# Performance work log

Measured on AMD Instinct MI355X. Metric: run time of the kernel, lower is better.

Reference implementation:

```python
import jax, jax.numpy as jnp
import numpy as np

N = 100000
NEG_SLOPE = 0.2

def setup_inputs() -> dict:
    key = jax.random.key(0)
    ks = jax.random.split(key, 12)
    F_in, H, C1, C2 = 128, 2, 64, 64
    E = 1600000
    x = jax.random.normal(ks[0], (N, F_in), dtype=jnp.float32)
    edge_index = jax.random.randint(ks[1], (2, E), 0, N, dtype=jnp.int32)
    s1 = 1.0 / np.sqrt(F_in)
    s2 = 1.0 / np.sqrt(H * C1)
    return {
        "x": x,
        "edge_index": edge_index,
        "W1": jax.random.normal(ks[2], (F_in, H * C1), dtype=jnp.float32) * s1,
        "att_src1": jax.random.normal(ks[3], (H, C1), dtype=jnp.float32) * s1,
        "att_dst1": jax.random.normal(ks[4], (H, C1), dtype=jnp.float32) * s1,
        "b1": jnp.zeros((H * C1,), dtype=jnp.float32),
        "W2": jax.random.normal(ks[5], (H * C1, C2), dtype=jnp.float32) * s2,
        "att_src2": jax.random.normal(ks[6], (1, C2), dtype=jnp.float32) * s2,
        "att_dst2": jax.random.normal(ks[7], (1, C2), dtype=jnp.float32) * s2,
        "b2": jnp.zeros((C2,), dtype=jnp.float32),
    }

def gat_conv(x, W, att_src, att_dst, bias, src, dst):
    heads, out_ch = att_src.shape
    h = (x @ W).reshape(-1, heads, out_ch)            # [N, H, C]
    a_s = jnp.einsum('nhc,hc->nh', h, att_src)         # [N, H]
    a_d = jnp.einsum('nhc,hc->nh', h, att_dst)
    e = jax.nn.leaky_relu(a_s[src] + a_d[dst], NEG_SLOPE)   # [E, H]
    m = jax.ops.segment_max(e, dst, num_segments=N)
    ex = jnp.exp(e - m[dst])
    denom = jax.ops.segment_sum(ex, dst, num_segments=N)
    alpha = ex / denom[dst]                            # segment softmax per dst node
    msg = h[src] * alpha[:, :, None]                   # [E, H, C]
    out = jax.ops.segment_sum(msg, dst, num_segments=N)
    return out.reshape(N, heads * out_ch) + bias

def reference(x, edge_index, W1, att_src1, att_dst1, b1, W2, att_src2, att_dst2, b2):
    # PyG GATConv default add_self_loops=True
    loops = jnp.arange(N, dtype=edge_index.dtype)
    src = jnp.concatenate([edge_index[0], loops])
    dst = jnp.concatenate([edge_index[1], loops])
    h1 = gat_conv(x, W1, att_src1, att_dst1, b1, src, dst)
    h1 = jax.nn.elu(h1)
    return gat_conv(h1, W2, att_src2, att_dst2, b2, src, dst)
```

## Files before the change

### kernel.cpp

```cpp
#include <hip/hip_runtime.h>
#include <hip/hip_bf16.h>
#include <hip/hip_fp16.h>
#include <math.h>

#define SLOPE 0.2f
#define CHUNK 4096
#define BCAP 6144

__host__ __device__ static inline int imin(int a, int b) { return a < b ? a : b; }

typedef _Float16 half8 __attribute__((ext_vector_type(8)));
typedef float f32x4 __attribute__((ext_vector_type(4)));

__device__ __forceinline__ unsigned fmap(float f) {
    unsigned u = __float_as_uint(f);
    return (u & 0x80000000u) ? ~u : (u | 0x80000000u);
}
__device__ __forceinline__ float funmap(unsigned u) {
    unsigned v = (u & 0x80000000u) ? (u & 0x7FFFFFFFu) : ~u;
    return __uint_as_float(v);
}

template<int HC, typename TIN>
__device__ __forceinline__
void gemm_att_body(int bid, int nblk,
                   const TIN* __restrict__ x, const float* __restrict__ W,
                   const float* __restrict__ att_s, const float* __restrict__ att_d,
                   __half* __restrict__ h, float* __restrict__ a_s,
                   float* __restrict__ a_d, unsigned* __restrict__ Ms, int N) {
    constexpr int H = HC / 64;
    constexpr int CT = HC / 16;
    __shared__ half8 blds[CT * 4 * 64];
    __shared__ half8 xlds[4 * 4 * 64];

    const int tid = threadIdx.x;
    const int lane = tid & 63;
    const int wid = tid >> 6;

    for (int u = tid; u < HC * 16; u += 256) {
        int col = u & (HC - 1), k8 = u / HC;
        half8 v;
#pragma unroll
        for (int j = 0; j < 8; ++j) v[j] = (_Float16)W[(k8 * 8 + j) * HC + col];
        blds[((col >> 4) * 4 + (k8 >> 2)) * 64 + (k8 & 3) * 16 + (col & 15)] = v;
    }

    float asv[CT], adv[CT];
#pragma unroll
    for (int ct = 0; ct < CT; ++ct) {
        asv[ct] = att_s[ct * 16 + (lane & 15)];
        adv[ct] = att_d[ct * 16 + (lane & 15)];
    }
    float ms0 = -INFINITY, ms1 = -INFINITY;

    const int ntiles = (N + 63) >> 6;
    for (int t = bid; t < ntiles; t += nblk) {
        const int row0 = t << 6;
        __syncthreads();
#pragma unroll
        for (int i = 0; i < 4; ++i) {
            int u = tid + 256 * i;
            int r = u >> 4, k8 = u & 15;
            int row = row0 + r;
            half8 v;
            if (row < N) {
                if (sizeof(TIN) == 4) {
                    float4 f0 = ((const float4*)x)[(size_t)row * 32 + k8 * 2];
                    float4 f1 = ((const float4*)x)[(size_t)row * 32 + k8 * 2 + 1];
                    v[0] = (_Float16)f0.x; v[1] = (_Float16)f0.y;
                    v[2] = (_Float16)f0.z; v[3] = (_Float16)f0.w;
                    v[4] = (_Float16)f1.x; v[5] = (_Float16)f1.y;
                    v[6] = (_Float16)f1.z; v[7] = (_Float16)f1.w;
                } else {
                    v = ((const half8*)x)[(size_t)row * 16 + k8];
                }
            } else {
#pragma unroll
                for (int j = 0; j < 8; ++j) v[j] = (_Float16)0.f;
            }
            xlds[((r >> 4) * 4 + (k8 >> 2)) * 64 + (k8 & 3) * 16 + (r & 15)] = v;
        }
        __syncthreads();

        f32x4 acc[CT];
#pragma unroll
        for (int ct = 0; ct < CT; ++ct) acc[ct] = f32x4{0.f, 0.f, 0.f, 0.f};
        half8 afrag[4];
#pragma unroll
        for (int s = 0; s < 4; ++s) afrag[s] = xlds[(wid * 4 + s) * 64 + lane];
#pragma unroll
        for (int ct = 0; ct < CT; ++ct)
#pragma unroll
            for (int s = 0; s < 4; ++s)
                acc[ct] = __builtin_amdgcn_mfma_f32_16x16x32_f16(
                    afrag[s], blds[(ct * 4 + s) * 64 + lane], acc[ct], 0, 0, 0);

#pragma unroll
        for (int q = 0; q < 4; ++q) {
            int row = row0 + wid * 16 + (lane >> 4) * 4 + q;
            bool ok = row < N;
#pragma unroll
            for (int ct = 0; ct < CT; ++ct)
                if (ok) h[(size_t)row * HC + ct * 16 + (lane & 15)] =
                    __float2half((float)acc[ct][q]);
            float vs0 = 0.f, vd0 = 0.f, vs1 = 0.f, vd1 = 0.f;
#pragma unroll
            for (int ct = 0; ct < CT; ++ct) {
                float a = acc[ct][q];
                if (H == 2 && ct >= CT / 2) { vs1 = fmaf(a, asv[ct], vs1); vd1 = fmaf(a, adv[ct], vd1); }
                else                        { vs0 = fmaf(a, asv[ct], vs0); vd0 = fmaf(a, adv[ct], vd0); }
            }
#pragma unroll
            for (int off = 1; off < 16; off <<= 1) {
                vs0 += __shfl_xor(vs0, off); vd0 += __shfl_xor(vd0, off);
                if (H == 2) { vs1 += __shfl_xor(vs1, off); vd1 += __shfl_xor(vd1, off); }
            }
            if (ok) {
                ms0 = fmaxf(ms0, vs0);
                if (H == 2) ms1 = fmaxf(ms1, vs1);
                if ((lane & 15) == 0) {
                    if (H == 2) {
                        ((float2*)a_s)[row] = make_float2(vs0, vs1);
                        ((float2*)a_d)[row] = make_float2(vd0, vd1);
                    } else {
                        a_s[row] = vs0;
                        a_d[row] = vd0;
                    }
                }
            }
        }
    }
#pragma unroll
    for (int off = 1; off < 64; off <<= 1) {
        ms0 = fmaxf(ms0, __shfl_xor(ms0, off));
        if (H == 2) ms1 = fmaxf(ms1, __shfl_xor(ms1, off));
    }
    if (lane == 0) {
        atomicMax(&Ms[0], fmap(ms0));
        if (H == 2) atomicMax(&Ms[1], fmap(ms1));
    }
}

__device__ __forceinline__
void bscatter_body(int bid, const int* __restrict__ ei, int E, int Etot,
                   int* __restrict__ bnext, unsigned* __restrict__ pairs, int nb) {
    __shared__ int lcnt[512];
    __shared__ int lbase[512];
    const int t = threadIdx.x;
    const int c0 = bid * CHUNK;
    const int lim = imin(CHUNK, Etot - c0);

    for (int i = t; i < nb; i += 256) lcnt[i] = 0;
    __syncthreads();
    for (int j = t; j < lim; j += 256) {
        int e = c0 + j;
        int dst = (e < E) ? ei[E + e] : (e - E);
        atomicAdd(&lcnt[dst >> 8], 1);
    }
    __syncthreads();
    for (int i = t; i < nb; i += 256) {
        int c = lcnt[i];
        lbase[i] = c ? atomicAdd(&bnext[i], c) : 0;
        lcnt[i] = 0;
    }
    __syncthreads();
    for (int j = t; j < lim; j += 256) {
        int e = c0 + j;
        int src = (e < E) ? ei[e] : (e - E);
        int dst = (e < E) ? ei[E + e] : (e - E);
        int b = dst >> 8;
        int off = atomicAdd(&lcnt[b], 1);
        pairs[(size_t)b * BCAP + lbase[b] + off] =
            ((unsigned)(dst & 255) << 24) | (unsigned)src;
    }
}

__global__ __launch_bounds__(256, 2)
void fat1_k(const int* __restrict__ ei, int E, int Etot,
            int* __restrict__ bnext, unsigned* __restrict__ pairs, int nb, int cb,
            const float* __restrict__ x, const float* __restrict__ W,
            const float* __restrict__ att_s, const float* __restrict__ att_d,
            __half* __restrict__ h, float* __restrict__ a_s,
            float* __restrict__ a_d, unsigned* __restrict__ Ms, int N, int gblk) {
    if ((int)blockIdx.x < cb)
        bscatter_body(blockIdx.x, ei, E, Etot, bnext, pairs, nb);
    else
        gemm_att_body<128, float>(blockIdx.x - cb, gblk, x, W, att_s, att_d,
                                  h, a_s, a_d, Ms, N);
}

__global__ __launch_bounds__(256, 2)
void gemm2_k(const __half* __restrict__ x, const float* __restrict__ W,
             const float* __restrict__ att_s, const float* __restrict__ att_d,
             __half* __restrict__ h, float* __restrict__ a_s,
             float* __restrict__ a_d, unsigned* __restrict__ Ms, int N) {
    gemm_att_body<64, __half>(blockIdx.x, gridDim.x, x, W, att_s, att_d,
                              h, a_s, a_d, Ms, N);
}

__global__ __launch_bounds__(512)
void bscan_k(const int* __restrict__ bnext, int* __restrict__ bbase,
             int* __restrict__ rowptr, int nb, int N, int Etot) {
    __shared__ int sm[512];
    int t = threadIdx.x;
    int v = (t < nb) ? bnext[t] : 0;
    sm[t] = v; __syncthreads();
    for (int off = 1; off < 512; off <<= 1) {
        int u = (t >= off) ? sm[t - off] : 0;
        __syncthreads();
        sm[t] += u;
        __syncthreads();
    }
    if (t < nb) bbase[t] = sm[t] - v;
    if (t == 0) rowptr[N] = Etot;
}

__global__ __launch_bounds__(256)
void fine_k(const unsigned* __restrict__ pairs, const int* __restrict__ bnext,
            const int* __restrict__ bbase, int* __restrict__ rowptr,
            int* __restrict__ colsrc, int N) {
    __shared__ int sm[256];
    __shared__ int lnext[256];
    const int b = blockIdx.x, t = threadIdx.x;
    const int cnt = bnext[b];
    const int gbase = bbase[b];
    const size_t pbase = (size_t)b * BCAP;

    lnext[t] = 0;
    __syncthreads();
    for (int i = t; i < cnt; i += 256)
        atomicAdd(&lnext[pairs[pbase + i] >> 24], 1);
    __syncthreads();
    int v = lnext[t];
    sm[t] = v; __syncthreads();
    for (int off = 1; off < 256; off <<= 1) {
        int u = (t >= off) ? sm[t - off] : 0;
        __syncthreads();
        sm[t] += u;
        __syncthreads();
    }
    int excl = sm[t] - v;
    int node = (b << 8) + t;
    if (node < N) rowptr[node] = gbase + excl;
    lnext[t] = excl;
    __syncthreads();
    for (int i = t; i < cnt; i += 256) {
        unsigned pr = pairs[pbase + i];
        int p = atomicAdd(&lnext[pr >> 24], 1);
        colsrc[gbase + p] = (int)(pr & 0xFFFFFFu);
    }
}

template<bool ELU>
__global__ __launch_bounds__(256)
void node_aggr2(const int* __restrict__ rowptr, const int* __restrict__ colsrc,
                const float* __restrict__ a_s, const float* __restrict__ a_d,
                const __half* __restrict__ h, const float* __restrict__ bias,
                const unsigned* __restrict__ Ms, __half* __restrict__ out, int N) {
    int gw = (blockIdx.x * 256 + threadIdx.x) >> 6;
    int lane = threadIdx.x & 63;
    int nw = (gridDim.x * 256) >> 6;
    const int g = lane >> 4;
    const int p = lane & 15;
    const float AS0 = funmap(Ms[0]);
    const float AS1 = funmap(Ms[1]);
    float4 bv0 = ((const float4*)bias)[p * 2];
    float4 bv1 = ((const float4*)bias)[p * 2 + 1];

    for (int n = gw; n < N; n += nw) {
        const int b = rowptr[n], deg = rowptr[n + 1] - b;
        const float2 adn = ((const float2*)a_d)[n];
        float M0 = AS0 + adn.x; M0 = M0 > 0.f ? M0 : SLOPE * M0;
        float M1 = AS1 + adn.y; M1 = M1 > 0.f ? M1 : SLOPE * M1;
        float4 acc0 = make_float4(0.f, 0.f, 0.f, 0.f);
        float4 acc1 = make_float4(0.f, 0.f, 0.f, 0.f);
        float den = 0.f;

        for (int c = 0; c < deg; c += 64) {
            int ii = c + lane;
            int src_r = 0;
            float w0_r = 0.f, w1_r = 0.f;
            if (ii < deg) {
                src_r = colsrc[b + ii];
                float2 as = ((const float2*)a_s)[src_r];
                float s0 = as.x + adn.x; s0 = s0 > 0.f ? s0 : SLOPE * s0;
                float s1 = as.y + adn.y; s1 = s1 > 0.f ? s1 : SLOPE * s1;
                w0_r = __expf(s0 - M0);
                w1_r = __expf(s1 - M1);
            }
            int lim = (deg - c < 64) ? (deg - c) : 64;
#pragma unroll 2
            for (int i = 0; i < lim; i += 4) {
                int e = i + g;
                int src = __shfl(src_r, e);
                float w0b = __shfl(w0_r, e);
                float w1b = __shfl(w1_r, e);
                float w = (p < 8) ? w0b : w1b;
                den += w;
                uint4 hv = ((const uint4*)h)[(size_t)src * 16 + p];
                float2 f0 = __half22float2(*(__half2*)&hv.x);
                float2 f1 = __half22float2(*(__half2*)&hv.y);
                float2 f2 = __half22float2(*(__half2*)&hv.z);
                float2 f3 = __half22float2(*(__half2*)&hv.w);
                acc0.x = fmaf(w, f0.x, acc0.x); acc0.y = fmaf(w, f0.y, acc0.y);
                acc0.z = fmaf(w, f1.x, acc0.z); acc0.w = fmaf(w, f1.y, acc0.w);
                acc1.x = fmaf(w, f2.x, acc1.x); acc1.y = fmaf(w, f2.y, acc1.y);
                acc1.z = fmaf(w, f3.x, acc1.z); acc1.w = fmaf(w, f3.y, acc1.w);
            }
        }
#pragma unroll
        for (int off = 16; off <= 32; off <<= 1) {
            acc0.x += __shfl_xor(acc0.x, off); acc0.y += __shfl_xor(acc0.y, off);
            acc0.z += __shfl_xor(acc0.z, off); acc0.w += __shfl_xor(acc0.w, off);
            acc1.x += __shfl_xor(acc1.x, off); acc1.y += __shfl_xor(acc1.y, off);
            acc1.z += __shfl_xor(acc1.z, off); acc1.w += __shfl_xor(acc1.w, off);
            den    += __shfl_xor(den, off);
        }
        if (lane < 16) {
            float inv = 1.f / den;
            float4 o0, o1;
            o0.x = acc0.x * inv + bv0.x; o0.y = acc0.y * inv + bv0.y;
            o0.z = acc0.z * inv + bv0.z; o0.w = acc0.w * inv + bv0.w;
            o1.x = acc1.x * inv + bv1.x; o1.y = acc1.y * inv + bv1.y;
            o1.z = acc1.z * inv + bv1.z; o1.w = acc1.w * inv + bv1.w;
            if (ELU) {
                o0.x = o0.x > 0.f ? o0.x : expm1f(o0.x);
                o0.y = o0.y > 0.f ? o0.y : expm1f(o0.y);
                o0.z = o0.z > 0.f ? o0.z : expm1f(o0.z);
                o0.w = o0.w > 0.f ? o0.w : expm1f(o0.w);
                o1.x = o1.x > 0.f ? o1.x : expm1f(o1.x);
                o1.y = o1.y > 0.f ? o1.y : expm1f(o1.y);
                o1.z = o1.z > 0.f ? o1.z : expm1f(o1.z);
                o1.w = o1.w > 0.f ? o1.w : expm1f(o1.w);
            }
            __half2 q0 = __floats2half2_rn(o0.x, o0.y);
            __half2 q1 = __floats2half2_rn(o0.z, o0.w);
            __half2 q2 = __floats2half2_rn(o1.x, o1.y);
            __half2 q3 = __floats2half2_rn(o1.z, o1.w);
            uint4 pk;
            pk.x = *(unsigned*)&q0; pk.y = *(unsigned*)&q1;
            pk.z = *(unsigned*)&q2; pk.w = *(unsigned*)&q3;
            ((uint4*)out)[(size_t)n * 16 + p] = pk;
        }
    }
}

__global__ __launch_bounds__(256)
void node_aggr1(const int* __restrict__ rowptr, const int* __restrict__ colsrc,
                const float* __restrict__ a_s, const float* __restrict__ a_d,
                const __half* __restrict__ h, const float* __restrict__ bias,
                const unsigned* __restrict__ Ms, float* __restrict__ out, int N) {
    int gw = (blockIdx.x * 256 + threadIdx.x) >> 6;
    int lane = threadIdx.x & 63;
    int nw = (gridDim.x * 256) >> 6;
    const int g = lane >> 3;
    const int p = lane & 7;
    const float AS = funmap(Ms[0]);
    float4 bv0 = ((const float4*)bias)[p * 2];
    float4 bv1 = ((const float4*)bias)[p * 2 + 1];

    for (int n = gw; n < N; n += nw) {
        const int b = rowptr[n], deg = rowptr[n + 1] - b;
        const float adn = a_d[n];
        float M = AS + adn; M = M > 0.f ? M : SLOPE * M;
        float den = 0.f;
        float4 acc0 = make_float4(0.f, 0.f, 0.f, 0.f);
        float4 acc1 = make_float4(0.f, 0.f, 0.f, 0.f);

        for (int c = 0; c < deg; c += 64) {
            int ii = c + lane;
            int src_r = 0;
            float w_r = 0.f;
            if (ii < deg) {
                src_r = colsrc[b + ii];
                float s = a_s[src_r] + adn;
                s = s > 0.f ? s : SLOPE * s;
                w_r = __expf(s - M);
            }
            int lim = (deg - c < 64) ? (deg - c) : 64;
#pragma unroll 2
            for (int i = 0; i < lim; i += 8) {
                int e = i + g;
                int src = __shfl(src_r, e);
                float w = __shfl(w_r, e);
                den += w;
                uint4 hv = ((const uint4*)h)[(size_t)src * 8 + p];
                float2 f0 = __half22float2(*(__half2*)&hv.x);
                float2 f1 = __half22float2(*(__half2*)&hv.y);
                float2 f2 = __half22float2(*(__half2*)&hv.z);
                float2 f3 = __half22float2(*(__half2*)&hv.w);
                acc0.x = fmaf(w, f0.x, acc0.x); acc0.y = fmaf(w, f0.y, acc0.y);
                acc0.z = fmaf(w, f1.x, acc0.z); acc0.w = fmaf(w, f1.y, acc0.w);
                acc1.x = fmaf(w, f2.x, acc1.x); acc1.y = fmaf(w, f2.y, acc1.y);
                acc1.z = fmaf(w, f3.x, acc1.z); acc1.w = fmaf(w, f3.y, acc1.w);
            }
        }
#pragma unroll
        for (int off = 8; off <= 32; off <<= 1) {
            acc0.x += __shfl_xor(acc0.x, off); acc0.y += __shfl_xor(acc0.y, off);
            acc0.z += __shfl_xor(acc0.z, off); acc0.w += __shfl_xor(acc0.w, off);
            acc1.x += __shfl_xor(acc1.x, off); acc1.y += __shfl_xor(acc1.y, off);
            acc1.z += __shfl_xor(acc1.z, off); acc1.w += __shfl_xor(acc1.w, off);
            den    += __shfl_xor(den, off);
        }
        if (lane < 8) {
            float inv = 1.f / den;
            float4 o0, o1;
            o0.x = acc0.x * inv + bv0.x; o0.y = acc0.y * inv + bv0.y;
            o0.z = acc0.z * inv + bv0.z; o0.w = acc0.w * inv + bv0.w;
            o1.x = acc1.x * inv + bv1.x; o1.y = acc1.y * inv + bv1.y;
            o1.z = acc1.z * inv + bv1.z; o1.w = acc1.w * inv + bv1.w;
            ((float4*)out)[(size_t)n * 16 + p * 2]     = o0;
            ((float4*)out)[(size_t)n * 16 + p * 2 + 1] = o1;
        }
    }
}

extern "C" void kernel_launch(void* const* d_in, const int* in_sizes, int n_in,
                              void* d_out, int out_size, void* d_ws, size_t ws_size,
                              hipStream_t stream) {
    const float* x   = (const float*)d_in[0];
    const int*   ei  = (const int*)d_in[1];
    const float* W1  = (const float*)d_in[2];
    const float* as1 = (const float*)d_in[3];
    const float* ad1 = (const float*)d_in[4];
    const float* b1  = (const float*)d_in[5];
    const float* W2  = (const float*)d_in[6];
    const float* as2 = (const float*)d_in[7];
    const float* ad2 = (const float*)d_in[8];
    const float* b2  = (const float*)d_in[9];
    float* out = (float*)d_out;

    const int N = out_size / 64;
    const int E = in_sizes[1] / 2;
    const int Etot = E + N;
    const int nb = (N + 255) >> 8;

    float* ws   = (float*)d_ws;
    __half* h1  = (__half*)ws;
    __half* h1e = (__half*)(ws + (size_t)N * 64);
    float* a_s1 = ws + (size_t)N * 128;
    float* a_d1 = a_s1 + (size_t)N * 2;
    float* a_s2 = a_d1 + (size_t)N * 2;
    float* a_d2 = a_s2 + (size_t)N;
    int* rowptr = (int*)(a_d2 + (size_t)N);
    int* bbase  = rowptr + (N + 1);
    int* bnext  = bbase + 513;
    unsigned* Ms = (unsigned*)(bnext + 512);
    int* colsrc = (int*)(Ms + 4);
    unsigned* pairs = (unsigned*)(colsrc + Etot);

    (void)hipMemsetAsync(bnext, 0, (512 + 4) * 4, stream);

    int cb = (Etot + CHUNK - 1) / CHUNK;
    const int GB = 512;

    fat1_k<<<dim3(cb + GB), dim3(256), 0, stream>>>(
        ei, E, Etot, bnext, pairs, nb, cb,
        x, W1, as1, ad1, h1, a_s1, a_d1, Ms, N, GB);
    bscan_k<<<dim3(1), dim3(512), 0, stream>>>(bnext, bbase, rowptr, nb, N, Etot);
    fine_k<<<dim3(nb), dim3(256), 0, stream>>>(pairs, bnext, bbase, rowptr, colsrc, N);

    int ab = imin((N + 3) / 4, 25000);

    node_aggr2<true><<<dim3(ab), dim3(256), 0, stream>>>(
        rowptr, colsrc, a_s1, a_d1, h1, b1, Ms, h1e, N);

    __half* h2 = h1;
    gemm2_k<<<dim3(512), dim3(256), 0, stream>>>(
        h1e, W2, as2, ad2, h2, a_s2, a_d2, Ms + 2, N);
    node_aggr1<<<dim3(ab), dim3(256), 0, stream>>>(
        rowptr, colsrc, a_s2, a_d2, h2, b2, Ms + 2, out, N);
}
```

Baseline: 276.8 us.

## Fold attention vectors into GEMM as extra MFMA column tile, drop x LDS staging

Precomputes W·att_src and W·att_dst per input feature into an extra column tile of the B operand, so attention logits come out of the MFMA instead of per-row FMAs and shuffle reductions. Each wave now loads its own 16-row A fragments straight from global memory instead of staging a 64-row tile through LDS with block barriers. Occupancy hints go from 2 to 4 blocks per CU and the GEMM grids double. Folding the attention vectors into the B operand rounds them to fp16 before accumulation, which slightly changes the precision of the attention logits.

```diff
diff --git a/kernel.cpp b/kernel.cpp
--- a/kernel.cpp
+++ b/kernel.cpp
@@ -30,12 +30,12 @@
                    float* __restrict__ a_d, unsigned* __restrict__ Ms, int N) {
     constexpr int H = HC / 64;
     constexpr int CT = HC / 16;
-    __shared__ half8 blds[CT * 4 * 64];
-    __shared__ half8 xlds[4 * 4 * 64];
+    __shared__ half8 blds[(CT + 1) * 4 * 64];
 
     const int tid = threadIdx.x;
     const int lane = tid & 63;
     const int wid = tid >> 6;
+    const int c15 = lane & 15;
 
     for (int u = tid; u < HC * 16; u += 256) {
         int col = u & (HC - 1), k8 = u / HC;
@@ -44,91 +44,93 @@
         for (int j = 0; j < 8; ++j) v[j] = (_Float16)W[(k8 * 8 + j) * HC + col];
         blds[((col >> 4) * 4 + (k8 >> 2)) * 64 + (k8 & 3) * 16 + (col & 15)] = v;
     }
-
-    float asv[CT], adv[CT];
-#pragma unroll
-    for (int ct = 0; ct < CT; ++ct) {
-        asv[ct] = att_s[ct * 16 + (lane & 15)];
-        adv[ct] = att_d[ct * 16 + (lane & 15)];
-    }
+    for (int u = tid; u < 4 * 64; u += 256) {
+        half8 z;
+#pragma unroll
+        for (int j = 0; j < 8; ++j) z[j] = (_Float16)0.f;
+        blds[CT * 4 * 64 + u] = z;
+    }
+    __syncthreads();
+    if (tid < 128) {
+        int k = tid;
+        float wa0 = 0.f, wd0 = 0.f, wa1 = 0.f, wd1 = 0.f;
+        for (int c = 0; c < HC; ++c) {
+            float wv = W[(size_t)k * HC + c];
+            float s = att_s[c], d = att_d[c];
+            if (H == 2 && c >= 64) { wa1 = fmaf(wv, s, wa1); wd1 = fmaf(wv, d, wd1); }
+            else                   { wa0 = fmaf(wv, s, wa0); wd0 = fmaf(wv, d, wd0); }
+        }
+        __half* eb = (__half*)&blds[CT * 4 * 64];
+        int fi = (k >> 5) * 64 + ((k >> 3) & 3) * 16;
+        int j = k & 7;
+        eb[(fi + 0) * 8 + j] = __float2half(wa0);
+        eb[(fi + 1) * 8 + j] = __float2half(wd0);
+        if (H == 2) {
+            eb[(fi + 2) * 8 + j] = __float2half(wa1);
+            eb[(fi + 3) * 8 + j] = __float2half(wd1);
+        }
+    }
+    __syncthreads();
+
     float ms0 = -INFINITY, ms1 = -INFINITY;
-
-    const int ntiles = (N + 63) >> 6;
-    for (int t = bid; t < ntiles; t += nblk) {
-        const int row0 = t << 6;
-        __syncthreads();
-#pragma unroll
-        for (int i = 0; i < 4; ++i) {
-            int u = tid + 256 * i;
-            int r = u >> 4, k8 = u & 15;
-            int row = row0 + r;
-            half8 v;
-            if (row < N) {
-                if (sizeof(TIN) == 4) {
-                    float4 f0 = ((const float4*)x)[(size_t)row * 32 + k8 * 2];
-                    float4 f1 = ((const float4*)x)[(size_t)row * 32 + k8 * 2 + 1];
-                    v[0] = (_Float16)f0.x; v[1] = (_Float16)f0.y;
-                    v[2] = (_Float16)f0.z; v[3] = (_Float16)f0.w;
-                    v[4] = (_Float16)f1.x; v[5] = (_Float16)f1.y;
-                    v[6] = (_Float16)f1.z; v[7] = (_Float16)f1.w;
-                } else {
-                    v = ((const half8*)x)[(size_t)row * 16 + k8];
-                }
+    const int ntiles = (N + 15) >> 4;
+    const int wtot = nblk * 4;
+    for (int t = bid * 4 + wid; t < ntiles; t += wtot) {
+        const int row0 = t << 4;
+        const int myrow = row0 + c15;
+        const int rcl = myrow < N ? myrow : N - 1;
+
+        half8 af[4];
+#pragma unroll
+        for (int s = 0; s < 4; ++s) {
+            int k0 = s * 32 + (lane >> 4) * 8;
+            if (sizeof(TIN) == 4) {
+                float4 f0 = ((const float4*)x)[(size_t)rcl * 32 + (k0 >> 2)];
+                float4 f1 = ((const float4*)x)[(size_t)rcl * 32 + (k0 >> 2) + 1];
+                af[s][0] = (_Float16)f0.x; af[s][1] = (_Float16)f0.y;
+                af[s][2] = (_Float16)f0.z; af[s][3] = (_Float16)f0.w;
+                af[s][4] = (_Float16)f1.x; af[s][5] = (_Float16)f1.y;
+                af[s][6] = (_Float16)f1.z; af[s][7] = (_Float16)f1.w;
             } else {
-#pragma unroll
-                for (int j = 0; j < 8; ++j) v[j] = (_Float16)0.f;
-            }
-            xlds[((r >> 4) * 4 + (k8 >> 2)) * 64 + (k8 & 3) * 16 + (r & 15)] = v;
-        }
-        __syncthreads();
-
-        f32x4 acc[CT];
-#pragma unroll
-        for (int ct = 0; ct < CT; ++ct) acc[ct] = f32x4{0.f, 0.f, 0.f, 0.f};
-        half8 afrag[4];
-#pragma unroll
-        for (int s = 0; s < 4; ++s) afrag[s] = xlds[(wid * 4 + s) * 64 + lane];
-#pragma unroll
-        for (int ct = 0; ct < CT; ++ct)
+                af[s] = ((const half8*)x)[(size_t)rcl * 16 + (k0 >> 3)];
+            }
+        }
+
+        f32x4 acc[CT + 1];
+#pragma unroll
+        for (int ct = 0; ct <= CT; ++ct) acc[ct] = f32x4{0.f, 0.f, 0.f, 0.f};
+#pragma unroll
+        for (int ct = 0; ct <= CT; ++ct)
 #pragma unroll
             for (int s = 0; s < 4; ++s)
                 acc[ct] = __builtin_amdgcn_mfma_f32_16x16x32_f16(
-                    afrag[s], blds[(ct * 4 + s) * 64 + lane], acc[ct], 0, 0, 0);
-
+                    af[s], blds[(ct * 4 + s) * 64 + lane], acc[ct], 0, 0, 0);
+
+        float msl = -INFINITY;
 #pragma unroll
         for (int q = 0; q < 4; ++q) {
-            int row = row0 + wid * 16 + (lane >> 4) * 4 + q;
+            int row = row0 + (lane >> 4) * 4 + q;
             bool ok = row < N;
 #pragma unroll
             for (int ct = 0; ct < CT; ++ct)
-                if (ok) h[(size_t)row * HC + ct * 16 + (lane & 15)] =
+                if (ok) h[(size_t)row * HC + ct * 16 + c15] =
                     __float2half((float)acc[ct][q]);
-            float vs0 = 0.f, vd0 = 0.f, vs1 = 0.f, vd1 = 0.f;
-#pragma unroll
-            for (int ct = 0; ct < CT; ++ct) {
-                float a = acc[ct][q];
-                if (H == 2 && ct >= CT / 2) { vs1 = fmaf(a, asv[ct], vs1); vd1 = fmaf(a, adv[ct], vd1); }
-                else                        { vs0 = fmaf(a, asv[ct], vs0); vd0 = fmaf(a, adv[ct], vd0); }
-            }
-#pragma unroll
-            for (int off = 1; off < 16; off <<= 1) {
-                vs0 += __shfl_xor(vs0, off); vd0 += __shfl_xor(vd0, off);
-                if (H == 2) { vs1 += __shfl_xor(vs1, off); vd1 += __shfl_xor(vd1, off); }
-            }
+            float ev = (float)acc[CT][q];
             if (ok) {
-                ms0 = fmaxf(ms0, vs0);
-                if (H == 2) ms1 = fmaxf(ms1, vs1);
-                if ((lane & 15) == 0) {
-                    if (H == 2) {
-                        ((float2*)a_s)[row] = make_float2(vs0, vs1);
-                        ((float2*)a_d)[row] = make_float2(vd0, vd1);
-                    } else {
-                        a_s[row] = vs0;
-                        a_d[row] = vd0;
-                    }
+                msl = fmaxf(msl, ev);
+                if (H == 2) {
+                    if      (c15 == 0) a_s[row * 2]     = ev;
+                    else if (c15 == 1) a_d[row * 2]     = ev;
+                    else if (c15 == 2) a_s[row * 2 + 1] = ev;
+                    else if (c15 == 3) a_d[row * 2 + 1] = ev;
+                } else {
+                    if      (c15 == 0) a_s[row] = ev;
+                    else if (c15 == 1) a_d[row] = ev;
                 }
             }
         }
+        if (c15 == 0) ms0 = fmaxf(ms0, msl);
+        if (H == 2 && c15 == 2) ms1 = fmaxf(ms1, msl);
     }
 #pragma unroll
     for (int off = 1; off < 64; off <<= 1) {
@@ -175,7 +177,7 @@
     }
 }
 
-__global__ __launch_bounds__(256, 2)
+__global__ __launch_bounds__(256, 4)
 void fat1_k(const int* __restrict__ ei, int E, int Etot,
             int* __restrict__ bnext, unsigned* __restrict__ pairs, int nb, int cb,
             const float* __restrict__ x, const float* __restrict__ W,
@@ -189,7 +191,7 @@
                                   h, a_s, a_d, Ms, N);
 }
 
-__global__ __launch_bounds__(256, 2)
+__global__ __launch_bounds__(256, 4)
 void gemm2_k(const __half* __restrict__ x, const float* __restrict__ W,
              const float* __restrict__ att_s, const float* __restrict__ att_d,
              __half* __restrict__ h, float* __restrict__ a_s,
@@ -453,7 +455,7 @@
     (void)hipMemsetAsync(bnext, 0, (512 + 4) * 4, stream);
 
     int cb = (Etot + CHUNK - 1) / CHUNK;
-    const int GB = 512;
+    const int GB = 1024;
 
     fat1_k<<<dim3(cb + GB), dim3(256), 0, stream>>>(
         ei, E, Etot, bnext, pairs, nb, cb,
@@ -467,7 +469,7 @@
         rowptr, colsrc, a_s1, a_d1, h1, b1, Ms, h1e, N);
 
     __half* h2 = h1;
-    gemm2_k<<<dim3(512), dim3(256), 0, stream>>>(
+    gemm2_k<<<dim3(1024), dim3(256), 0, stream>>>(
         h1e, W2, as2, ad2, h2, a_s2, a_d2, Ms + 2, N);
     node_aggr1<<<dim3(ab), dim3(256), 0, stream>>>(
         rowptr, colsrc, a_s2, a_d2, h2, b2, Ms + 2, out, N);
```

Measured after the change: 374.9 us. 35.4% more time.
